# Performance work log

Measured on AMD Instinct MI355X. Metric: run time of the kernel, lower is better.

## Reference

```python
import jax, jax.numpy as jnp
import numpy as np

B, N, D, H, HD, HID, RP_HID = 4, 512, 1024, 16, 64, 4096, 64
EPS = 1e-5


def _ln(h, g, b):
    mu = h.mean(-1, keepdims=True)
    var = h.var(-1, keepdims=True)
    return (h - mu) / jnp.sqrt(var + EPS) * g + b


def setup_inputs() -> dict:
    key = jax.random.key(0)
    ks = jax.random.split(key, 24)
    s = 0.05
    return {
        "x": jax.random.normal(ks[0], (B, N, D), jnp.float32),
        "t_emb": jax.random.normal(ks[1], (B, D), jnp.float32),
        "rel_pos_matrix": jax.random.normal(ks[2], (B, N, N, 2), jnp.float32),
        "agent_mask": jax.random.randint(ks[3], (B, N), 0, 2).astype(jnp.int32),
        # adaLN modulation: Linear(D, 6D)
        "w_ada": jax.random.normal(ks[4], (6 * D, D), jnp.float32) * s,
        "b_ada": jnp.zeros((6 * D,), jnp.float32),
        # LayerNorms
        "g1": jnp.ones((D,), jnp.float32),
        "beta1": jnp.zeros((D,), jnp.float32),
        "g2": jnp.ones((D,), jnp.float32),
        "beta2": jnp.zeros((D,), jnp.float32),
        # attention qkv / proj
        "w_qkv": jax.random.normal(ks[5], (3 * D, D), jnp.float32) * s,
        "b_qkv": jnp.zeros((3 * D,), jnp.float32),
        "w_proj": jax.random.normal(ks[6], (D, D), jnp.float32) * s,
        "b_proj": jnp.zeros((D,), jnp.float32),
        # rel-pos bias MLP: Linear(2,64) -> ReLU -> Linear(64,H)
        "w_rp1": jax.random.normal(ks[7], (RP_HID, 2), jnp.float32) * s,
        "b_rp1": jnp.zeros((RP_HID,), jnp.float32),
        "w_rp2": jax.random.normal(ks[8], (H, RP_HID), jnp.float32) * s,
        "b_rp2": jnp.zeros((H,), jnp.float32),
        # MLP: Linear(D, HID) -> GELU -> Linear(HID, D)
        "w_fc1": jax.random.normal(ks[9], (HID, D), jnp.float32) * s,
        "b_fc1": jnp.zeros((HID,), jnp.float32),
        "w_fc2": jax.random.normal(ks[10], (D, HID), jnp.float32) * s,
        "b_fc2": jnp.zeros((D,), jnp.float32),
    }


def reference(x, t_emb, rel_pos_matrix, agent_mask,
              w_ada, b_ada, g1, beta1, w_qkv, b_qkv, w_proj, b_proj,
              w_rp1, b_rp1, w_rp2, b_rp2, g2, beta2,
              w_fc1, b_fc1, w_fc2, b_fc2):
    b, n, d = x.shape
    # adaLN: SiLU -> Linear -> 6 chunks of [B, D]
    mod = jax.nn.silu(t_emb) @ w_ada.T + b_ada
    shift_s, scale_s, gate_s, shift_m, scale_m, gate_m = jnp.split(mod, 6, axis=1)

    # ---- spatial attention branch ----
    xn = _ln(x, g1, beta1) * (1.0 + scale_s[:, None, :]) + shift_s[:, None, :]
    qkv = (xn @ w_qkv.T + b_qkv).reshape(b, n, 3, H, HD)
    q, k, v = jnp.moveaxis(qkv, 2, 0)  # each [B, N, H, HD]
    attn = jnp.einsum('bnhd,bmhd->bhnm', q, k) * (HD ** -0.5)
    # relative-position bias MLP: [B,N,N,2] -> [B,N,N,H] -> [B,H,N,N]
    bias = jax.nn.relu(rel_pos_matrix @ w_rp1.T + b_rp1) @ w_rp2.T + b_rp2
    attn = attn + bias.transpose(0, 3, 1, 2)
    mask = agent_mask.astype(bool)[:, None, None, :]  # key-side mask [B,1,1,N]
    attn = jnp.where(mask, attn, -jnp.inf)
    p = jax.nn.softmax(attn, axis=-1)
    out = jnp.einsum('bhnm,bmhd->bnhd', p, v).reshape(b, n, d)
    out = out @ w_proj.T + b_proj
    x = x + gate_s[:, None, :] * out

    # ---- gated MLP branch ----
    xn = _ln(x, g2, beta2) * (1.0 + scale_m[:, None, :]) + shift_m[:, None, :]
    h = jax.nn.gelu(xn @ w_fc1.T + b_fc1, approximate=False)
    x = x + gate_m[:, None, :] * (h @ w_fc2.T + b_fc2)
    return x
```

## Files before the change

### kernel.cpp

```cpp
#include <hip/hip_runtime.h>


#define B_ 4
#define N_ 512
#define D_ 1024
#define H_ 16
#define HID_ 4096
#define M_ (B_*N_)

typedef unsigned short u16;
typedef __attribute__((ext_vector_type(8))) short bf16x8;
typedef __attribute__((ext_vector_type(4))) float f32x4;

__device__ __forceinline__ float b2f(u16 u){
  union { unsigned int i; float f; } x; x.i = ((unsigned int)u) << 16; return x.f;
}
__device__ __forceinline__ u16 f2b(float f){
  unsigned int u = __float_as_uint(f);
  return (u16)((u + 0x7fffu + ((u >> 16) & 1u)) >> 16);
}

__device__ __forceinline__ void gload16(const u16* __restrict__ g, u16* l){
#if defined(__has_builtin) && __has_builtin(__builtin_amdgcn_global_load_lds)
  __builtin_amdgcn_global_load_lds(
      (const __attribute__((address_space(1))) unsigned int*)g,
      (__attribute__((address_space(3))) unsigned int*)l, 16, 0, 0);
#else
  *(uint4*)l = *(const uint4*)g;
#endif
}

__global__ __launch_bounds__(256) void k_pre(
    const float* __restrict__ w_qkv, u16* __restrict__ wqkvb,
    const float* __restrict__ w_proj, u16* __restrict__ wprojb,
    const float* __restrict__ w_fc1, u16* __restrict__ wfc1b,
    const float* __restrict__ w_fc2, u16* __restrict__ wfc2b,
    const float* __restrict__ t_emb, const float* __restrict__ w_ada,
    const float* __restrict__ b_ada, float* __restrict__ mod,
    const float* __restrict__ rel, const int* __restrict__ amask,
    const float* __restrict__ w_rp1, const float* __restrict__ b_rp1,
    const float* __restrict__ w_rp2, const float* __restrict__ b_rp2,
    u16* __restrict__ biasbuf)
{
  __shared__ __align__(16) char smem[48448];
  int blk = blockIdx.x, tid = threadIdx.x;
  int w = tid >> 6, lane = tid & 63, ln = lane & 15, quad = lane >> 4;

  if (blk < 1536){
    float* st = (float*)smem;
    #pragma unroll
    for (int i = 0; i < 16; i++){
      int idx = tid + i*256;
      float x = t_emb[idx];
      st[idx] = x / (1.f + __expf(-x));
    }

    const float* s; u16* d; size_t base;
    if      (blk <  384){ s = w_qkv;  d = wqkvb;  base = (size_t)blk*8192; }
    else if (blk <  512){ s = w_proj; d = wprojb; base = (size_t)(blk-384)*8192; }
    else if (blk < 1024){ s = w_fc1;  d = wfc1b;  base = (size_t)(blk-512)*8192; }
    else                { s = w_fc2;  d = wfc2b;  base = (size_t)(blk-1024)*8192; }
    float4 a[4], bq[4];
    #pragma unroll
    for (int it=0; it<4; it++){
      size_t i = base + (size_t)it*2048 + (size_t)tid*8;
      a[it]  = *(const float4*)(s+i);
      bq[it] = *(const float4*)(s+i+4);
    }

    int j = blk*4 + w;
    const float* wr = w_ada + (size_t)j*D_ + 4*lane;
    float4 wv[4];
    #pragma unroll
    for (int i=0;i<4;i++) wv[i] = *(const float4*)(wr + i*256);

    #pragma unroll
    for (int it=0; it<4; it++){
      size_t i = base + (size_t)it*2048 + (size_t)tid*8;
      u16 o[8] = {f2b(a[it].x),f2b(a[it].y),f2b(a[it].z),f2b(a[it].w),
                  f2b(bq[it].x),f2b(bq[it].y),f2b(bq[it].z),f2b(bq[it].w)};
      *(uint4*)(d+i) = *(const uint4*)o;
    }

    __syncthreads();

    float acc[B_] = {};
    #pragma unroll
    for (int i=0;i<4;i++){
      int p = 4*lane + 256*i;
      #pragma unroll
      for (int b=0;b<B_;b++){
        float4 sv = *(const float4*)&st[b*D_ + p];
        acc[b] += wv[i].x*sv.x + wv[i].y*sv.y + wv[i].z*sv.z + wv[i].w*sv.w;
      }
    }
    #pragma unroll
    for (int b=0;b<B_;b++)
      #pragma unroll
      for (int o=32;o>0;o>>=1) acc[b] += __shfl_down(acc[b], o);
    if (lane == 0){
      float bj = b_ada[j];
      #pragma unroll
      for (int b=0;b<B_;b++) mod[b*6*D_ + j] = acc[b] + bj;
    }
    return;
  }

  int idx = blk - 1536;
  int mh = idx & 1, n = (idx >> 1) & 511, b = idx >> 10;
  u16*  Hs  = (u16*)smem;
  u16*  Bs  = (u16*)(smem + 36864);
  u16*  w2s = (u16*)(smem + 36864 + 8704);
  float* b2s = (float*)(smem + 36864+8704+2304);
  u16*  msk = (u16*)(smem + 36864+8704+2304+64);

  for (int i = tid; i < 1024; i += 256) w2s[(i>>6)*72 + (i&63)] = f2b(w_rp2[i]);
  if (tid < 16) b2s[tid] = b_rp2[tid];
  msk[tid] = (u16)(amask[b*N_ + mh*256 + tid] != 0);

  {
    float2 r01 = *(const float2*)(rel + ((size_t)((b*N_ + n)*N_) + mh*256 + tid)*2);
    u16 hv[64];
    #pragma unroll
    for (int j=0;j<64;j++){
      float t = w_rp1[2*j]*r01.x + w_rp1[2*j+1]*r01.y + b_rp1[j];
      hv[j] = f2b(t > 0.f ? t : 0.f);
    }
    uint4* dst = (uint4*)&Hs[tid*72];
    #pragma unroll
    for (int c=0;c<8;c++) dst[c] = *(const uint4*)&hv[c*8];
  }
  __syncthreads();

  bf16x8 af0 = *(const bf16x8*)&w2s[ln*72 + quad*8];
  bf16x8 af1 = *(const bf16x8*)&w2s[ln*72 + 32 + quad*8];

  #pragma unroll
  for (int t=0; t<4; t++){
    int mt = w*4 + t;
    bf16x8 bf0 = *(const bf16x8*)&Hs[(mt*16+ln)*72 + quad*8];
    bf16x8 bf1 = *(const bf16x8*)&Hs[(mt*16+ln)*72 + 32 + quad*8];
    f32x4 c = {};
    c = __builtin_amdgcn_mfma_f32_16x16x32_bf16(af0, bf0, c, 0,0,0);
    c = __builtin_amdgcn_mfma_f32_16x16x32_bf16(af1, bf1, c, 0,0,0);
    bool valid = msk[mt*16 + ln] != 0;
    #pragma unroll
    for (int i=0;i<4;i++){
      int h = quad*4 + i;
      float val = valid ? (c[i] + b2s[h]) : -1e30f;
      Bs[h*272 + mt*16 + ln] = f2b(val);
    }
  }
  __syncthreads();

  #pragma unroll
  for (int it=0; it<8; it++){
    int idx2 = it*256 + tid;
    int r = idx2 >> 7, cc = idx2 & 127;
    size_t rb = (((size_t)(b*H_ + r)*N_) + n)*N_ + mh*256;
    ((unsigned int*)(biasbuf + rb))[cc] = ((const unsigned int*)(Bs + r*272))[cc];
  }
}

__global__ __launch_bounds__(256) void k_lnmod(const float* __restrict__ xin,
    const float* __restrict__ g, const float* __restrict__ be,
    const float* __restrict__ mod, int shift_idx, int scale_idx,
    u16* __restrict__ xn)
{
  int row = blockIdx.x;
  int b = row >> 9;
  float v[4]; float s = 0.f, s2 = 0.f;
  #pragma unroll
  for (int i=0;i<4;i++){
    float x = xin[(size_t)row*D_ + threadIdx.x + i*256];
    v[i] = x; s += x; s2 += x*x;
  }
  #pragma unroll
  for (int o=32;o>0;o>>=1){ s += __shfl_down(s,o); s2 += __shfl_down(s2,o); }
  __shared__ float rs[4], rs2[4];
  int w = threadIdx.x >> 6;
  if ((threadIdx.x & 63)==0){ rs[w]=s; rs2[w]=s2; }
  __syncthreads();
  s = rs[0]+rs[1]+rs[2]+rs[3]; s2 = rs2[0]+rs2[1]+rs2[2]+rs2[3];
  float mu = s * (1.f/D_);
  float var = s2 * (1.f/D_) - mu*mu;
  float rstd = rsqrtf(var + 1e-5f);
  const float* mrow = mod + b*6*D_;
  #pragma unroll
  for (int i=0;i<4;i++){
    int d = threadIdx.x + i*256;
    float xg = (v[i]-mu)*rstd*g[d] + be[d];
    xn[(size_t)row*D_ + d] = f2b(xg * (1.f + mrow[scale_idx*D_ + d]) + mrow[shift_idx*D_ + d]);
  }
}

enum { EPI_PLAIN=0, EPI_GELU=1 };

template<int EPI>
__global__ __launch_bounds__(256) void k_gemm64(const u16* __restrict__ A,
    const u16* __restrict__ W, const float* __restrict__ Wb, int K, int ldc,
    u16* __restrict__ o_u16)
{
  __shared__ __align__(16) u16 Al[64*64];
  __shared__ __align__(16) u16 Wl[128*64];
  int row0 = blockIdx.y*64, col0 = blockIdx.x*128;
  int tid = threadIdx.x;
  int w = tid >> 6, lane = tid & 63, ln = lane & 15, quad = lane >> 4;
  int wy = w >> 1, wx = w & 1;
  int srow = tid >> 3;
  int schunk = (tid & 7) ^ (srow & 7);
  const u16* Ag = A + (size_t)(row0 + srow)*K + schunk*8;
  const u16* Wg = W + (size_t)(col0 + srow)*K + schunk*8;
  int aoff[2][2], woff[4][2];
  #pragma unroll
  for (int ms=0; ms<2; ms++){
    int r = 32*wy + 16*ms + ln;
    #pragma unroll
    for (int kk=0; kk<2; kk++)
      aoff[ms][kk] = r*64 + (((kk*4+quad) ^ (ln&7))*8);
  }
  #pragma unroll
  for (int ns=0; ns<4; ns++){
    int r = 64*wx + 16*ns + ln;
    #pragma unroll
    for (int kk=0; kk<2; kk++)
      woff[ns][kk] = r*64 + (((kk*4+quad) ^ (ln&7))*8);
  }
  f32x4 acc[2][4] = {};
  for (int k0 = 0; k0 < K; k0 += 64){
    gload16(Ag + k0,                  Al + tid*8);
    gload16(Ag + k0 + (size_t)32*K,   Al + 2048 + tid*8);
    #pragma unroll
    for (int i=0;i<4;i++)
      gload16(Wg + k0 + (size_t)(32*i)*K, Wl + i*2048 + tid*8);
    __syncthreads();
    #pragma unroll
    for (int kk=0; kk<2; kk++){
      bf16x8 af[2], bfr[4];
      #pragma unroll
      for (int ms=0; ms<2; ms++) af[ms]  = *(const bf16x8*)&Al[aoff[ms][kk]];
      #pragma unroll
      for (int ns=0; ns<4; ns++) bfr[ns] = *(const bf16x8*)&Wl[woff[ns][kk]];
      #pragma unroll
      for (int ms=0; ms<2; ms++)
        #pragma unroll
        for (int ns=0; ns<4; ns++)
          acc[ms][ns] = __builtin_amdgcn_mfma_f32_16x16x32_bf16(af[ms], bfr[ns], acc[ms][ns], 0,0,0);
    }
    __syncthreads();
  }
  #pragma unroll
  for (int ms=0; ms<2; ms++){
    #pragma unroll
    for (int ns=0; ns<4; ns++){
      int c = col0 + 64*wx + 16*ns + ln;
      float wb = Wb[c];
      #pragma unroll
      for (int i=0;i<4;i++){
        int r = row0 + 32*wy + 16*ms + quad*4 + i;
        float val = acc[ms][ns][i] + wb;
        if (EPI == EPI_GELU) val = 0.5f*val*(1.f + erff(val*0.70710678f));
        o_u16[(size_t)r*ldc + c] = f2b(val);
      }
    }
  }
}

__global__ __launch_bounds__(256) void k_gemm(const u16* __restrict__ A,
    const u16* __restrict__ W, int K, int Kslice, int ldc,
    u16* __restrict__ part)
{
  __shared__ __align__(16) u16 Al[128*64];
  __shared__ __align__(16) u16 Wl[128*64];
  int row0 = blockIdx.y*128, col0 = blockIdx.x*128;
  int tid = threadIdx.x;
  int w = tid >> 6, lane = tid & 63, ln = lane & 15, quad = lane >> 4;
  int wy = w >> 1, wx = w & 1;
  int srow = tid >> 3;
  int schunk = (tid & 7) ^ (srow & 7);
  const u16* Ag = A + (size_t)(row0 + srow)*K + schunk*8;
  const u16* Wg = W + (size_t)(col0 + srow)*K + schunk*8;
  int aoff[4][2], woff[4][2];
  #pragma unroll
  for (int ms=0; ms<4; ms++){
    int r = 64*wy + 16*ms + ln;
    #pragma unroll
    for (int kk=0; kk<2; kk++)
      aoff[ms][kk] = r*64 + (((kk*4+quad) ^ (ln&7))*8);
  }
  #pragma unroll
  for (int ns=0; ns<4; ns++){
    int r = 64*wx + 16*ns + ln;
    #pragma unroll
    for (int kk=0; kk<2; kk++)
      woff[ns][kk] = r*64 + (((kk*4+quad) ^ (ln&7))*8);
  }
  f32x4 acc[4][4] = {};
  int kbeg = blockIdx.z * Kslice;
  for (int k0 = kbeg; k0 < kbeg + Kslice; k0 += 64){
    #pragma unroll
    for (int i=0;i<4;i++){
      gload16(Ag + k0 + (size_t)(32*i)*K, Al + i*2048 + tid*8);
      gload16(Wg + k0 + (size_t)(32*i)*K, Wl + i*2048 + tid*8);
    }
    __syncthreads();
    #pragma unroll
    for (int kk=0; kk<2; kk++){
      bf16x8 af[4], bfr[4];
      #pragma unroll
      for (int ms=0; ms<4; ms++) af[ms]  = *(const bf16x8*)&Al[aoff[ms][kk]];
      #pragma unroll
      for (int ns=0; ns<4; ns++) bfr[ns] = *(const bf16x8*)&Wl[woff[ns][kk]];
      #pragma unroll
      for (int ms=0; ms<4; ms++)
        #pragma unroll
        for (int ns=0; ns<4; ns++)
          acc[ms][ns] = __builtin_amdgcn_mfma_f32_16x16x32_bf16(af[ms], bfr[ns], acc[ms][ns], 0,0,0);
    }
    __syncthreads();
  }
  u16* pbase = part + (size_t)blockIdx.z*M_*ldc;
  #pragma unroll
  for (int ms=0; ms<4; ms++){
    #pragma unroll
    for (int ns=0; ns<4; ns++){
      int c = col0 + 64*wx + 16*ns + ln;
      #pragma unroll
      for (int i=0;i<4;i++){
        int r = row0 + 64*wy + 16*ms + quad*4 + i;
        pbase[(size_t)r*ldc + c] = f2b(acc[ms][ns][i]);
      }
    }
  }
}

template<int GIDX>
__global__ __launch_bounds__(256) void k_red4(const u16* __restrict__ part,
    const float* __restrict__ Wb, const float* __restrict__ mod,
    const float* __restrict__ resid, float* __restrict__ outp)
{
  size_t i = ((size_t)blockIdx.x*256 + threadIdx.x)*4;
  int c = (int)(i & 1023); int r = (int)(i >> 10); int b = r >> 9;
  uint2 a0 = *(const uint2*)(part + i);
  uint2 a1 = *(const uint2*)(part + (size_t)M_*D_ + i);
  uint2 a2 = *(const uint2*)(part + (size_t)2*M_*D_ + i);
  uint2 a3 = *(const uint2*)(part + (size_t)3*M_*D_ + i);
  float4 pv;
  pv.x = b2f((u16)(a0.x&0xffff)) + b2f((u16)(a1.x&0xffff)) + b2f((u16)(a2.x&0xffff)) + b2f((u16)(a3.x&0xffff));
  pv.y = b2f((u16)(a0.x>>16))    + b2f((u16)(a1.x>>16))    + b2f((u16)(a2.x>>16))    + b2f((u16)(a3.x>>16));
  pv.z = b2f((u16)(a0.y&0xffff)) + b2f((u16)(a1.y&0xffff)) + b2f((u16)(a2.y&0xffff)) + b2f((u16)(a3.y&0xffff));
  pv.w = b2f((u16)(a0.y>>16))    + b2f((u16)(a1.y>>16))    + b2f((u16)(a2.y>>16))    + b2f((u16)(a3.y>>16));
  float4 x4 = *(const float4*)(resid + i);
  float4 bi = *(const float4*)(Wb + c);
  float4 g4 = *(const float4*)(mod + b*6*D_ + GIDX*D_ + c);
  float4 o;
  o.x = x4.x + g4.x*(pv.x + bi.x);
  o.y = x4.y + g4.y*(pv.y + bi.y);
  o.z = x4.z + g4.z*(pv.z + bi.z);
  o.w = x4.w + g4.w*(pv.w + bi.w);
  *(float4*)(outp + i) = o;
}

__global__ __launch_bounds__(256) void k_redln(const u16* __restrict__ proj,
    const float* __restrict__ mod, const float* __restrict__ resid,
    const float* __restrict__ g, const float* __restrict__ be,
    float* __restrict__ xm, u16* __restrict__ xn)
{
  int row = blockIdx.x, b = row >> 9, tid = threadIdx.x;
  size_t i = (size_t)row*D_ + tid*4;
  int c = tid*4;
  uint2 a0 = *(const uint2*)(proj + i);
  float4 pv;
  pv.x = b2f((u16)(a0.x&0xffff));
  pv.y = b2f((u16)(a0.x>>16));
  pv.z = b2f((u16)(a0.y&0xffff));
  pv.w = b2f((u16)(a0.y>>16));
  float4 x4 = *(const float4*)(resid + i);
  float4 g4 = *(const float4*)(mod + b*6*D_ + 2*D_ + c);
  float4 mid;
  mid.x = x4.x + g4.x*pv.x;
  mid.y = x4.y + g4.y*pv.y;
  mid.z = x4.z + g4.z*pv.z;
  mid.w = x4.w + g4.w*pv.w;
  *(float4*)(xm + i) = mid;
  float s = mid.x+mid.y+mid.z+mid.w;
  float s2 = mid.x*mid.x+mid.y*mid.y+mid.z*mid.z+mid.w*mid.w;
  #pragma unroll
  for (int o=32;o>0;o>>=1){ s += __shfl_down(s,o); s2 += __shfl_down(s2,o); }
  __shared__ float rs[4], rs2[4];
  int w = tid >> 6;
  if ((tid & 63)==0){ rs[w]=s; rs2[w]=s2; }
  __syncthreads();
  s = rs[0]+rs[1]+rs[2]+rs[3]; s2 = rs2[0]+rs2[1]+rs2[2]+rs2[3];
  float mu = s * (1.f/D_);
  float var = s2 * (1.f/D_) - mu*mu;
  float rstd = rsqrtf(var + 1e-5f);
  const float* mrow = mod + b*6*D_;
  float4 gg = *(const float4*)(g + c);
  float4 bb = *(const float4*)(be + c);
  float4 sc = *(const float4*)(mrow + 4*D_ + c);
  float4 sh = *(const float4*)(mrow + 3*D_ + c);
  u16 o[4];
  o[0] = f2b(((mid.x-mu)*rstd*gg.x + bb.x)*(1.f+sc.x) + sh.x);
  o[1] = f2b(((mid.y-mu)*rstd*gg.y + bb.y)*(1.f+sc.y) + sh.y);
  o[2] = f2b(((mid.z-mu)*rstd*gg.z + bb.z)*(1.f+sc.z) + sh.z);
  o[3] = f2b(((mid.w-mu)*rstd*gg.w + bb.w)*(1.f+sc.w) + sh.w);
  *(uint2*)(xn + i) = *(const uint2*)o;
}

__global__ __launch_bounds__(256) void k_attn(const u16* __restrict__ qkv,
    const u16* __restrict__ biasbuf, u16* __restrict__ attn_out)
{
  __shared__ __align__(16) u16 Qs[64*72];
  __shared__ __align__(16) u16 Ks[64*72];
  __shared__ __align__(16) u16 Vt[64*72];
  __shared__ __align__(16) u16 Ps[4*16*72];
  int nt = blockIdx.x, h = blockIdx.y, b = blockIdx.z;
  int n0 = nt*64;
  int tid = threadIdx.x;
  int w = tid >> 6, lane = tid & 63, ln = lane & 15, quad = lane >> 4;

  {
    int row = tid >> 2, cb = (tid & 3)*16;
    const u16* src = qkv + (size_t)(b*N_ + n0 + row)*3072 + h*64 + cb;
    uint4 q0 = *(const uint4*)src, q1 = *(const uint4*)(src+8);
    uint4* dst = (uint4*)&Qs[row*72 + cb];
    dst[0] = q0; dst[1] = q1;
  }
  __syncthreads();
  bf16x8 qf[2];
  qf[0] = *(const bf16x8*)&Qs[(16*w+ln)*72 + quad*8];
  qf[1] = *(const bf16x8*)&Qs[(16*w+ln)*72 + 32 + quad*8];

  f32x4 oacc[4] = {};
  float rmax[4] = {-3e38f,-3e38f,-3e38f,-3e38f};
  float rsum[4] = {0.f,0.f,0.f,0.f};
  const u16* bp = biasbuf + (((size_t)(b*H_ + h)*N_) + n0 + 16*w)*N_ + ln;

  for (int mt = 0; mt < 8; mt++){
    __syncthreads();
    {
      int r = tid >> 2, cb = (tid & 3)*16;
      const u16* kp = qkv + (size_t)(b*N_ + mt*64 + r)*3072 + 1024 + h*64 + cb;
      uint4 k0 = *(const uint4*)kp, k1 = *(const uint4*)(kp+8);
      uint4* kd = (uint4*)&Ks[r*72 + cb];
      kd[0] = k0; kd[1] = k1;
      const u16* vp = qkv + (size_t)(b*N_ + mt*64 + r)*3072 + 2048 + h*64 + cb;
      uint4 v0 = *(const uint4*)vp, v1 = *(const uint4*)(vp+8);
      u16 ve[16];
      *(uint4*)&ve[0] = v0; *(uint4*)&ve[8] = v1;
      #pragma unroll
      for (int j=0;j<16;j++) Vt[(cb+j)*72 + r] = ve[j];
    }
    __syncthreads();

    u16 bl[4][4];
    #pragma unroll
    for (int cs=0; cs<4; cs++)
      #pragma unroll
      for (int i=0;i<4;i++)
        bl[cs][i] = bp[(size_t)(quad*4+i)*N_ + mt*64 + 16*cs];

    f32x4 s[4];
    #pragma unroll
    for (int cs=0; cs<4; cs++){
      bf16x8 k0f = *(const bf16x8*)&Ks[(16*cs+ln)*72 + quad*8];
      bf16x8 k1f = *(const bf16x8*)&Ks[(16*cs+ln)*72 + 32 + quad*8];
      f32x4 z = {};
      z = __builtin_amdgcn_mfma_f32_16x16x32_bf16(qf[0], k0f, z, 0,0,0);
      z = __builtin_amdgcn_mfma_f32_16x16x32_bf16(qf[1], k1f, z, 0,0,0);
      s[cs] = z;
    }
    #pragma unroll
    for (int cs=0; cs<4; cs++)
      #pragma unroll
      for (int i=0;i<4;i++)
        s[cs][i] = s[cs][i]*0.125f + b2f(bl[cs][i]);

    #pragma unroll
    for (int i=0;i<4;i++){
      float tm = fmaxf(fmaxf(s[0][i], s[1][i]), fmaxf(s[2][i], s[3][i]));
      #pragma unroll
      for (int o=1;o<16;o<<=1) tm = fmaxf(tm, __shfl_xor(tm, o));
      float nm = fmaxf(rmax[i], tm);
      float alpha = __expf(rmax[i] - nm);
      rmax[i] = nm;
      float ps = 0.f;
      #pragma unroll
      for (int cs=0; cs<4; cs++){
        float p = __expf(s[cs][i] - nm);
        s[cs][i] = p; ps += p;
      }
      #pragma unroll
      for (int o=1;o<16;o<<=1) ps += __shfl_xor(ps, o);
      rsum[i] = rsum[i]*alpha + ps;
      #pragma unroll
      for (int ds=0; ds<4; ds++) oacc[ds][i] *= alpha;
    }

    #pragma unroll
    for (int cs=0; cs<4; cs++)
      #pragma unroll
      for (int i=0;i<4;i++)
        Ps[w*1152 + (quad*4+i)*72 + 16*cs + ln] = f2b(s[cs][i]);

    bf16x8 pf0 = *(const bf16x8*)&Ps[w*1152 + ln*72 + quad*8];
    bf16x8 pf1 = *(const bf16x8*)&Ps[w*1152 + ln*72 + 32 + quad*8];
    #pragma unroll
    for (int ds=0; ds<4; ds++){
      bf16x8 v0f = *(const bf16x8*)&Vt[(16*ds+ln)*72 + quad*8];
      bf16x8 v1f = *(const bf16x8*)&Vt[(16*ds+ln)*72 + 32 + quad*8];
      oacc[ds] = __builtin_amdgcn_mfma_f32_16x16x32_bf16(pf0, v0f, oacc[ds], 0,0,0);
      oacc[ds] = __builtin_amdgcn_mfma_f32_16x16x32_bf16(pf1, v1f, oacc[ds], 0,0,0);
    }
  }

  #pragma unroll
  for (int i=0;i<4;i++){
    float inv = 1.f / rsum[i];
    int r = b*N_ + n0 + 16*w + quad*4 + i;
    #pragma unroll
    for (int ds=0; ds<4; ds++)
      attn_out[(size_t)r*D_ + h*64 + 16*ds + ln] = f2b(oacc[ds][i]*inv);
  }
}

extern "C" void kernel_launch(void* const* d_in, const int* in_sizes, int n_in,
                              void* d_out, int out_size, void* d_ws, size_t ws_size,
                              hipStream_t stream) {
  const float* x      = (const float*)d_in[0];
  const float* t_emb  = (const float*)d_in[1];
  const float* rel    = (const float*)d_in[2];
  const int*   amask  = (const int*)d_in[3];
  const float* w_ada  = (const float*)d_in[4];
  const float* b_ada  = (const float*)d_in[5];
  const float* g1     = (const float*)d_in[6];
  const float* beta1  = (const float*)d_in[7];
  const float* g2     = (const float*)d_in[8];
  const float* beta2  = (const float*)d_in[9];
  const float* w_qkv  = (const float*)d_in[10];
  const float* b_qkv  = (const float*)d_in[11];
  const float* w_proj = (const float*)d_in[12];
  const float* b_proj = (const float*)d_in[13];
  const float* w_rp1  = (const float*)d_in[14];
  const float* b_rp1  = (const float*)d_in[15];
  const float* w_rp2  = (const float*)d_in[16];
  const float* b_rp2  = (const float*)d_in[17];
  const float* w_fc1  = (const float*)d_in[18];
  const float* b_fc1  = (const float*)d_in[19];
  const float* w_fc2  = (const float*)d_in[20];
  const float* b_fc2  = (const float*)d_in[21];
  float* outp = (float*)d_out;

  const size_t MB = 1u<<20;
  char* wsb = (char*)d_ws;
  float* mod   = (float*)(wsb);
  u16*  xn     = (u16*) (wsb + 131072);
  float* xm    = (float*)(wsb + 131072 + 4*MB);
  u16*  wqkvb  = (u16*) (wsb + 131072 + 12*MB);
  u16*  wprojb = (u16*) (wsb + 131072 + 18*MB);
  u16*  wfc1b  = (u16*) (wsb + 131072 + 20*MB);
  u16*  wfc2b  = (u16*) (wsb + 131072 + 28*MB);
  u16*  qkvb   = (u16*) (wsb + 131072 + 36*MB);
  u16*  biasb  = (u16*) (wsb + 131072 + 48*MB);
  u16*  hb     = (u16*) (wsb + 131072 + 80*MB);
  u16*  parts  = (u16*) (wsb + 131072 + 96*MB);

  k_pre<<<5632, 256, 0, stream>>>(
      w_qkv, wqkvb, w_proj, wprojb, w_fc1, wfc1b, w_fc2, wfc2b,
      t_emb, w_ada, b_ada, mod,
      rel, amask, w_rp1, b_rp1, w_rp2, b_rp2, biasb);
  k_lnmod<<<M_, 256, 0, stream>>>(x, g1, beta1, mod, 0, 1, xn);
  k_gemm64<EPI_PLAIN><<<dim3(3072/128, M_/64), 256, 0, stream>>>(
      xn, wqkvb, b_qkv, D_, 3072, qkvb);
  k_attn<<<dim3(8, H_, B_), 256, 0, stream>>>(qkvb, biasb, xn);
  k_gemm64<EPI_PLAIN><<<dim3(D_/128, M_/64), 256, 0, stream>>>(
      xn, wprojb, b_proj, D_, D_, parts);
  k_redln<<<M_, 256, 0, stream>>>(parts, mod, x, g2, beta2, xm, xn);
  k_gemm64<EPI_GELU><<<dim3(HID_/128, M_/64), 256, 0, stream>>>(
      xn, wfc1b, b_fc1, D_, HID_, hb);
  k_gemm<<<dim3(D_/128, M_/128, 4), 256, 0, stream>>>(
      hb, wfc2b, HID_, HID_/4, D_, parts);
  k_red4<5><<<2048, 256, 0, stream>>>(parts, b_fc2, mod, xm, outp);
}
```

Baseline: 326.8 us.

## Compute rel-pos hidden activations in registers and interleave pre-kernel block roles

The rel-pos bias path now builds each lane's slice of the hidden ReLU layer and the second-layer weights directly in registers, in MFMA fragment layout. This removes the LDS staging of the 64-wide hidden tile, the weights and the mask, plus one barrier, and shrinks shared memory from about 48KB to 16KB so more blocks fit per CU. Block indices are remapped so weight-conversion/adaLN blocks and bias blocks interleave (3 of every 11), mixing memory-heavy and compute-heavy work across the grid. The cost is more registers per lane and redundant per-lane loads of small weights from global/cache.

```diff
diff --git a/kernel.cpp b/kernel.cpp
--- a/kernel.cpp
+++ b/kernel.cpp
@@ -42,11 +42,13 @@
     const float* __restrict__ w_rp2, const float* __restrict__ b_rp2,
     u16* __restrict__ biasbuf)
 {
-  __shared__ __align__(16) char smem[48448];
+  __shared__ __align__(16) char smem[16384];
   int blk = blockIdx.x, tid = threadIdx.x;
   int w = tid >> 6, lane = tid & 63, ln = lane & 15, quad = lane >> 4;
-
-  if (blk < 1536){
+  int g = blk / 11, r = blk % 11;
+
+  if (r < 3){
+    int cblk = g*3 + r;
     float* st = (float*)smem;
     #pragma unroll
     for (int i = 0; i < 16; i++){
@@ -56,10 +58,10 @@
     }
 
     const float* s; u16* d; size_t base;
-    if      (blk <  384){ s = w_qkv;  d = wqkvb;  base = (size_t)blk*8192; }
-    else if (blk <  512){ s = w_proj; d = wprojb; base = (size_t)(blk-384)*8192; }
-    else if (blk < 1024){ s = w_fc1;  d = wfc1b;  base = (size_t)(blk-512)*8192; }
-    else                { s = w_fc2;  d = wfc2b;  base = (size_t)(blk-1024)*8192; }
+    if      (cblk <  384){ s = w_qkv;  d = wqkvb;  base = (size_t)cblk*8192; }
+    else if (cblk <  512){ s = w_proj; d = wprojb; base = (size_t)(cblk-384)*8192; }
+    else if (cblk < 1024){ s = w_fc1;  d = wfc1b;  base = (size_t)(cblk-512)*8192; }
+    else                 { s = w_fc2;  d = wfc2b;  base = (size_t)(cblk-1024)*8192; }
     float4 a[4], bq[4];
     #pragma unroll
     for (int it=0; it<4; it++){
@@ -68,7 +70,7 @@
       bq[it] = *(const float4*)(s+i+4);
     }
 
-    int j = blk*4 + w;
+    int j = cblk*4 + w;
     const float* wr = w_ada + (size_t)j*D_ + 4*lane;
     float4 wv[4];
     #pragma unroll
@@ -106,48 +108,62 @@
     return;
   }
 
-  int idx = blk - 1536;
+  int idx = g*8 + (r - 3);
   int mh = idx & 1, n = (idx >> 1) & 511, b = idx >> 10;
-  u16*  Hs  = (u16*)smem;
-  u16*  Bs  = (u16*)(smem + 36864);
-  u16*  w2s = (u16*)(smem + 36864 + 8704);
-  float* b2s = (float*)(smem + 36864+8704+2304);
-  u16*  msk = (u16*)(smem + 36864+8704+2304+64);
-
-  for (int i = tid; i < 1024; i += 256) w2s[(i>>6)*72 + (i&63)] = f2b(w_rp2[i]);
-  if (tid < 16) b2s[tid] = b_rp2[tid];
-  msk[tid] = (u16)(amask[b*N_ + mh*256 + tid] != 0);
-
-  {
-    float2 r01 = *(const float2*)(rel + ((size_t)((b*N_ + n)*N_) + mh*256 + tid)*2);
-    u16 hv[64];
-    #pragma unroll
-    for (int j=0;j<64;j++){
-      float t = w_rp1[2*j]*r01.x + w_rp1[2*j+1]*r01.y + b_rp1[j];
-      hv[j] = f2b(t > 0.f ? t : 0.f);
-    }
-    uint4* dst = (uint4*)&Hs[tid*72];
-    #pragma unroll
-    for (int c=0;c<8;c++) dst[c] = *(const uint4*)&hv[c*8];
-  }
-  __syncthreads();
-
-  bf16x8 af0 = *(const bf16x8*)&w2s[ln*72 + quad*8];
-  bf16x8 af1 = *(const bf16x8*)&w2s[ln*72 + 32 + quad*8];
+  u16* Bs = (u16*)smem;
+
+  const float* w2p = w_rp2 + ln*64 + quad*8;
+  float4 a0 = *(const float4*)(w2p);
+  float4 a1 = *(const float4*)(w2p+4);
+  float4 a2 = *(const float4*)(w2p+32);
+  float4 a3 = *(const float4*)(w2p+36);
+  u16 afe[16] = {f2b(a0.x),f2b(a0.y),f2b(a0.z),f2b(a0.w),
+                 f2b(a1.x),f2b(a1.y),f2b(a1.z),f2b(a1.w),
+                 f2b(a2.x),f2b(a2.y),f2b(a2.z),f2b(a2.w),
+                 f2b(a3.x),f2b(a3.y),f2b(a3.z),f2b(a3.w)};
+  bf16x8 af0 = *(const bf16x8*)&afe[0];
+  bf16x8 af1 = *(const bf16x8*)&afe[8];
+
+  float w1l[16], w1h[16], b1l[8], b1h[8];
+  *(float4*)&w1l[0]  = *(const float4*)(w_rp1 + quad*16);
+  *(float4*)&w1l[4]  = *(const float4*)(w_rp1 + quad*16 + 4);
+  *(float4*)&w1l[8]  = *(const float4*)(w_rp1 + quad*16 + 8);
+  *(float4*)&w1l[12] = *(const float4*)(w_rp1 + quad*16 + 12);
+  *(float4*)&w1h[0]  = *(const float4*)(w_rp1 + 64 + quad*16);
+  *(float4*)&w1h[4]  = *(const float4*)(w_rp1 + 64 + quad*16 + 4);
+  *(float4*)&w1h[8]  = *(const float4*)(w_rp1 + 64 + quad*16 + 8);
+  *(float4*)&w1h[12] = *(const float4*)(w_rp1 + 64 + quad*16 + 12);
+  *(float4*)&b1l[0]  = *(const float4*)(b_rp1 + quad*8);
+  *(float4*)&b1l[4]  = *(const float4*)(b_rp1 + quad*8 + 4);
+  *(float4*)&b1h[0]  = *(const float4*)(b_rp1 + 32 + quad*8);
+  *(float4*)&b1h[4]  = *(const float4*)(b_rp1 + 32 + quad*8 + 4);
+  float b2v[4];
+  #pragma unroll
+  for (int i=0;i<4;i++) b2v[i] = b_rp2[quad*4 + i];
 
   #pragma unroll
   for (int t=0; t<4; t++){
     int mt = w*4 + t;
-    bf16x8 bf0 = *(const bf16x8*)&Hs[(mt*16+ln)*72 + quad*8];
-    bf16x8 bf1 = *(const bf16x8*)&Hs[(mt*16+ln)*72 + 32 + quad*8];
+    int m = mh*256 + mt*16 + ln;
+    float2 r01 = *(const float2*)(rel + ((size_t)((b*N_ + n)*N_) + m)*2);
+    bool valid = amask[b*N_ + m] != 0;
+    u16 hv[16];
+    #pragma unroll
+    for (int j2=0;j2<8;j2++){
+      float hl = w1l[2*j2]*r01.x + w1l[2*j2+1]*r01.y + b1l[j2];
+      hv[j2]   = f2b(hl > 0.f ? hl : 0.f);
+      float hh = w1h[2*j2]*r01.x + w1h[2*j2+1]*r01.y + b1h[j2];
+      hv[8+j2] = f2b(hh > 0.f ? hh : 0.f);
+    }
+    bf16x8 bf0 = *(const bf16x8*)&hv[0];
+    bf16x8 bf1 = *(const bf16x8*)&hv[8];
     f32x4 c = {};
     c = __builtin_amdgcn_mfma_f32_16x16x32_bf16(af0, bf0, c, 0,0,0);
     c = __builtin_amdgcn_mfma_f32_16x16x32_bf16(af1, bf1, c, 0,0,0);
-    bool valid = msk[mt*16 + ln] != 0;
     #pragma unroll
     for (int i=0;i<4;i++){
       int h = quad*4 + i;
-      float val = valid ? (c[i] + b2s[h]) : -1e30f;
+      float val = valid ? (c[i] + b2v[i]) : -1e30f;
       Bs[h*272 + mt*16 + ln] = f2b(val);
     }
   }
@@ -156,9 +172,9 @@
   #pragma unroll
   for (int it=0; it<8; it++){
     int idx2 = it*256 + tid;
-    int r = idx2 >> 7, cc = idx2 & 127;
-    size_t rb = (((size_t)(b*H_ + r)*N_) + n)*N_ + mh*256;
-    ((unsigned int*)(biasbuf + rb))[cc] = ((const unsigned int*)(Bs + r*272))[cc];
+    int rr = idx2 >> 7, cc = idx2 & 127;
+    size_t rb = (((size_t)(b*H_ + rr)*N_) + n)*N_ + mh*256;
+    ((unsigned int*)(biasbuf + rb))[cc] = ((const unsigned int*)(Bs + rr*272))[cc];
   }
 }
 
```

Result: faster. 313.5 us (-4.1%).
